# Kernel optimization log

Measured on AMD Instinct MI355X. Metric: run time of the kernel, lower is better.

## Reference

```python
import jax, jax.numpy as jnp
import numpy as np

B, N_TOTAL, IN_CH, N_SUB, E, OUT_CH = 4096, 500, 8, 77, 400, 2
EPS = 1e-12


def _glorot(key, shape, scale=0.05):
    return jax.random.normal(key, shape, dtype=jnp.float32) * scale


def setup_inputs() -> dict:
    key = jax.random.key(0)
    ks = jax.random.split(key, 16)
    x = jax.random.normal(ks[0], (B, N_TOTAL, IN_CH), dtype=jnp.float32)
    n_id = jax.random.randint(ks[1], (N_SUB,), 0, N_TOTAL)
    edge_index = jax.random.randint(ks[2], (2, E), 0, N_SUB)
    return {
        "x": x, "n_id": n_id, "edge_index": edge_index,
        # SAGEConv weights: concat doubles the input dim
        "W1": _glorot(ks[3], (2 * IN_CH, 64)), "b1": jnp.zeros((64,), jnp.float32),
        "W2": _glorot(ks[4], (2 * 64, 256)),   "b2": jnp.zeros((256,), jnp.float32),
        "W3": _glorot(ks[5], (2 * 256, 512)),  "b3": jnp.zeros((512,), jnp.float32),
        # MLP head
        "L1w": _glorot(ks[6], (512 * N_SUB, 1024), 0.01), "L1b": jnp.zeros((1024,), jnp.float32),
        "L2w": _glorot(ks[7], (1024, 218)), "L2b": jnp.zeros((218,), jnp.float32),
        "L3w": _glorot(ks[8], (218, OUT_CH)), "L3b": jnp.zeros((OUT_CH,), jnp.float32),
    }


def sage_conv(x, edge_index, W, b):
    # x: [B, N_SUB, C]; edge_index: [2, E], local ids in [0, N_SUB)
    # PyG<=1.3 SAGEConv: remove self loops, add self loops, mean aggregate,
    # concat [x, aggr], linear, L2 normalize.
    src, dst = edge_index[0], edge_index[1]
    valid = (src != dst)
    vmask = valid.astype(x.dtype)
    msgs = x[:, src, :] * vmask[None, :, None]                       # [B, E, C]
    seg = jax.vmap(lambda m: jax.ops.segment_sum(m, dst, num_segments=N_SUB))(msgs)
    counts = jax.ops.segment_sum(vmask, dst, num_segments=N_SUB)     # [N_SUB]
    aggr = (seg + x) / (counts + 1.0)[None, :, None]                 # self loop included
    h = jnp.concatenate([x, aggr], axis=-1) @ W + b
    norm = jnp.linalg.norm(h, axis=-1, keepdims=True)
    return h / jnp.maximum(norm, EPS)


def reference(x, n_id, edge_index, W1, b1, W2, b2, W3, b3,
              L1w, L1b, L2w, L2b, L3w, L3b):
    xt = x[:, n_id, :]                                               # [B, 77, 8]
    xt = jax.nn.relu(sage_conv(xt, edge_index, W1, b1))              # [B, 77, 64]
    xt = jax.nn.relu(sage_conv(xt, edge_index, W2, b2))              # [B, 77, 256]
    xt = jax.nn.relu(sage_conv(xt, edge_index, W3, b3))              # [B, 77, 512]
    xt = xt.reshape(xt.shape[0], -1)                                 # [B, 39424]
    xt = jax.nn.relu(xt @ L1w + L1b)
    xt = jax.nn.relu(xt @ L2w + L2b)
    return xt @ L3w + L3b                                            # [B, 2]
```

## Files before the change

### kernel.cpp

```cpp
#include <hip/hip_runtime.h>
#include <hip/hip_bf16.h>
#include <stdint.h>

typedef unsigned short u16;
typedef __attribute__((ext_vector_type(8))) short bf16x8_t;
typedef __attribute__((ext_vector_type(4))) float f32x4_t;

#define B_SZ   4096
#define N_TOT  500
#define IN_CH  8
#define NS     77
#define NE     400
#define L2_OUT 218

#define AS1C(p) ((const __attribute__((address_space(1))) void*)(p))
#define AS3(p)  ((__attribute__((address_space(3))) void*)(p))

__device__ inline u16 f2b(float f) {
  union { float f; uint32_t u; } v; v.f = f;
  uint32_t r = v.u + 0x7FFFu + ((v.u >> 16) & 1u);
  return (u16)(r >> 16);
}
__device__ inline float b2f(u16 h) {
  union { uint32_t u; float f; } v; v.u = ((uint32_t)h) << 16; return v.f;
}

__global__ void k_setup(const int* __restrict__ ei, int* __restrict__ coff,
                        int* __restrict__ csrc, float* __restrict__ inv) {
  if (threadIdx.x != 0 || blockIdx.x != 0) return;
  int cnt[NS], cur[NS];
  for (int i = 0; i < NS; ++i) cnt[i] = 0;
  const int* src = ei; const int* dst = ei + NE;
  for (int e = 0; e < NE; ++e) if (src[e] != dst[e]) cnt[dst[e]]++;
  int acc = 0;
  for (int i = 0; i < NS; ++i) {
    coff[i] = acc; cur[i] = acc; acc += cnt[i];
    inv[i] = 1.0f / (float)(cnt[i] + 1);
  }
  coff[NS] = acc;
  for (int e = 0; e < NE; ++e) if (src[e] != dst[e]) csrc[cur[dst[e]]++] = src[e];
}

__global__ void k_wt(const float* __restrict__ W, u16* __restrict__ Wt,
                     int K, int Nsrc, int Ndst) {
  __shared__ float t[32][33];
  int nk = K / 32;
  int bk = blockIdx.x % nk, bn = blockIdx.x / nk;
  int r = threadIdx.x >> 3, c4 = (threadIdx.x & 7) * 4;
  int gn = bn * 32 + c4;
  const float* src = &W[(size_t)(bk * 32 + r) * Nsrc + gn];
  if (gn + 3 < Nsrc) {
    float4 v = *(const float4*)src;
    t[r][c4] = v.x; t[r][c4+1] = v.y; t[r][c4+2] = v.z; t[r][c4+3] = v.w;
  } else {
    #pragma unroll
    for (int j = 0; j < 4; ++j) t[r][c4 + j] = (gn + j < Nsrc) ? src[j] : 0.f;
  }
  __syncthreads();
  ushort4 o;
  o.x = f2b(t[c4+0][r]); o.y = f2b(t[c4+1][r]);
  o.z = f2b(t[c4+2][r]); o.w = f2b(t[c4+3][r]);
  *(ushort4*)&Wt[(size_t)(bn * 32 + r) * K + bk * 32 + c4] = o;
}

__global__ __launch_bounds__(256)
void k_front(const float* __restrict__ x, const int* __restrict__ nid,
             const float* __restrict__ W1, const float* __restrict__ b1,
             const int* __restrict__ coff, const int* __restrict__ csrc,
             const float* __restrict__ invc,
             u16* __restrict__ h1, u16* __restrict__ ag1) {
  __shared__ float Ws[16 * 64];
  __shared__ float bs[64];
  __shared__ float xs[NS * 8];
  __shared__ float ac[NS * 16];
  __shared__ u16  hn[NS * 64];
  __shared__ int soff[NS + 1];
  __shared__ int ssrc[NE];
  __shared__ float sinv[NS];
  __shared__ int snid[NS];
  const int b = blockIdx.x, t = threadIdx.x;

  ((float4*)Ws)[t] = ((const float4*)W1)[t];
  if (t < 64) bs[t] = b1[t];
  if (t < NS) { snid[t] = nid[t]; sinv[t] = invc[t]; }
  if (t < NS + 1) soff[t] = coff[t];
  for (int i = t; i < NE; i += 256) ssrc[i] = csrc[i];
  __syncthreads();

  if (t < 2 * NS) {
    int i = t >> 1, p = t & 1;
    float4 v = *(const float4*)(x + ((size_t)b * N_TOT + snid[i]) * IN_CH + p * 4);
    *(float4*)&xs[i * 8 + p * 4] = v;
  }
  __syncthreads();

  if (t < NS) {
    float s[8];
    #pragma unroll
    for (int c = 0; c < 8; ++c) { s[c] = xs[t * 8 + c]; ac[t * 16 + c] = s[c]; }
    for (int e = soff[t]; e < soff[t + 1]; ++e) {
      int sb = ssrc[e] * 8;
      #pragma unroll
      for (int c = 0; c < 8; ++c) s[c] += xs[sb + c];
    }
    float iv = sinv[t];
    #pragma unroll
    for (int c = 0; c < 8; ++c) ac[t * 16 + 8 + c] = s[c] * iv;
  }
  __syncthreads();

  const int w = t >> 6, lane = t & 63;
  for (int i = w; i < NS; i += 4) {
    float acc = bs[lane];
    #pragma unroll
    for (int k = 0; k < 16; ++k) acc += ac[i * 16 + k] * Ws[k * 64 + lane];
    float ss = acc * acc;
    #pragma unroll
    for (int d = 1; d < 64; d <<= 1) ss += __shfl_xor(ss, d);
    float rn = 1.0f / fmaxf(sqrtf(ss), 1e-12f);
    u16 hv = f2b(fmaxf(acc * rn, 0.f));
    hn[i * 64 + lane] = hv;
    h1[((size_t)b * NS + i) * 64 + lane] = hv;
  }
  __syncthreads();
  for (int i = w; i < NS; i += 4) {
    float s = b2f(hn[i * 64 + lane]);
    for (int e = soff[i]; e < soff[i + 1]; ++e) s += b2f(hn[ssrc[e] * 64 + lane]);
    ag1[((size_t)b * NS + i) * 64 + lane] = f2b(s * sinv[i]);
  }
}

template<int C>
__global__ __launch_bounds__(256)
void k_norm_aggr(u16* __restrict__ h, u16* __restrict__ ag,
                 const int* __restrict__ coff, const int* __restrict__ csrc,
                 const float* __restrict__ invc) {
  __shared__ u16 sh[NS * C];
  __shared__ int soff[NS + 1];
  __shared__ int ssrc[NE];
  __shared__ float sinv[NS];
  const int b = blockIdx.x, t = threadIdx.x;
  const ushort4* hb4 = (const ushort4*)(h + (size_t)b * NS * C);
  ushort4* sh4 = (ushort4*)sh;
  for (int i4 = t; i4 < NS * C / 4; i4 += 256) sh4[i4] = hb4[i4];
  for (int i = t; i < NS + 1; i += 256) soff[i] = coff[i];
  for (int i = t; i < NE; i += 256) ssrc[i] = csrc[i];
  for (int i = t; i < NS; i += 256) sinv[i] = invc[i];
  __syncthreads();
  const int w = t >> 6, lane = t & 63;
  constexpr int PER = C / 64;
  ushort4* hb4o = (ushort4*)(h + (size_t)b * NS * C);
  for (int i = w; i < NS; i += 4) {
    float v[PER]; float ss = 0.f;
    #pragma unroll
    for (int p = 0; p < PER / 4; ++p) {
      ushort4 r = *(ushort4*)&sh[i * C + lane * PER + p * 4];
      v[p*4+0] = b2f(r.x); v[p*4+1] = b2f(r.y); v[p*4+2] = b2f(r.z); v[p*4+3] = b2f(r.w);
    }
    #pragma unroll
    for (int p = 0; p < PER; ++p) ss += v[p] * v[p];
    #pragma unroll
    for (int d = 1; d < 64; d <<= 1) ss += __shfl_xor(ss, d);
    float rn = 1.0f / fmaxf(sqrtf(ss), 1e-12f);
    #pragma unroll
    for (int p = 0; p < PER / 4; ++p) {
      ushort4 o;
      o.x = f2b(fmaxf(v[p*4+0] * rn, 0.f)); o.y = f2b(fmaxf(v[p*4+1] * rn, 0.f));
      o.z = f2b(fmaxf(v[p*4+2] * rn, 0.f)); o.w = f2b(fmaxf(v[p*4+3] * rn, 0.f));
      *(ushort4*)&sh[i * C + lane * PER + p * 4] = o;
      hb4o[(i * C + lane * PER + p * 4) / 4] = o;
    }
  }
  __syncthreads();
  ushort4* ab4 = (ushort4*)(ag + (size_t)b * NS * C);
  for (int i = w; i < NS; i += 4) {
    #pragma unroll
    for (int p = 0; p < PER / 4; ++p) {
      int c0 = lane * PER + p * 4;
      ushort4 sv = *(ushort4*)&sh[i * C + c0];
      float s0 = b2f(sv.x), s1 = b2f(sv.y), s2 = b2f(sv.z), s3 = b2f(sv.w);
      for (int e = soff[i]; e < soff[i + 1]; ++e) {
        ushort4 nv = *(ushort4*)&sh[ssrc[e] * C + c0];
        s0 += b2f(nv.x); s1 += b2f(nv.y); s2 += b2f(nv.z); s3 += b2f(nv.w);
      }
      float iv = sinv[i];
      ushort4 o; o.x = f2b(s0 * iv); o.y = f2b(s1 * iv); o.z = f2b(s2 * iv); o.w = f2b(s3 * iv);
      ab4[(i * C + c0) / 4] = o;
    }
  }
}

template<int C>
__global__ void k_normrelu(u16* __restrict__ h) {
  const int row = blockIdx.x * 4 + (threadIdx.x >> 6);
  const int lane = threadIdx.x & 63;
  constexpr int PER = C / 64;
  u16* hr = h + (size_t)row * C;
  float v[PER];
  #pragma unroll
  for (int p = 0; p < PER / 4; ++p) {
    ushort4 r = *(const ushort4*)(hr + lane * PER + p * 4);
    v[p*4+0] = b2f(r.x); v[p*4+1] = b2f(r.y); v[p*4+2] = b2f(r.z); v[p*4+3] = b2f(r.w);
  }
  float ss = 0.f;
  #pragma unroll
  for (int j = 0; j < PER; ++j) ss += v[j] * v[j];
  #pragma unroll
  for (int d = 1; d < 64; d <<= 1) ss += __shfl_xor(ss, d);
  float rn = 1.0f / fmaxf(sqrtf(ss), 1e-12f);
  #pragma unroll
  for (int p = 0; p < PER / 4; ++p) {
    ushort4 o;
    o.x = f2b(fmaxf(v[p*4+0] * rn, 0.f)); o.y = f2b(fmaxf(v[p*4+1] * rn, 0.f));
    o.z = f2b(fmaxf(v[p*4+2] * rn, 0.f)); o.w = f2b(fmaxf(v[p*4+3] * rn, 0.f));
    *(ushort4*)(hr + lane * PER + p * 4) = o;
  }
}

template<int MODE, bool CONCAT>
__global__ __launch_bounds__(256)
void k_mfma(const u16* __restrict__ A, const u16* __restrict__ A2,
            const u16* __restrict__ Bt, const float* __restrict__ bias,
            void* __restrict__ Cv, int N, int K, int CIN,
            int kPerSplit, int Mtot, int NCOLS) {
  __shared__ u16 As[2][128 * 32];
  __shared__ u16 Bs[2][128 * 32];
  const int t = threadIdx.x;
  const int gx = gridDim.x, gy = gridDim.y;
  const int nwg = gx * gy;
  const int orig = blockIdx.y * gx + blockIdx.x;
  const int q = nwg >> 3, r8 = nwg & 7;
  const int xcd = orig & 7, jj = orig >> 3;
  const int swzb = (xcd < r8 ? xcd * (q + 1) : r8 * (q + 1) + (xcd - r8) * q) + jj;
  const int mt_i = swzb / gy, nt_i = swzb - mt_i * gy;
  const int row0 = mt_i * 128, col0 = nt_i * 128;
  const int split = blockIdx.z;
  const int kbeg = split * kPerSplit;
  const int w = t >> 6, l = t & 63;
  const int wm = w >> 1, wn = w & 1;
  const int lr = l & 15, ls = l >> 4;
  const int s_row = t >> 2;
  const int s_c = ((t & 3) ^ ((t >> 3) & 3)) * 8;
  const int lsw = (ls ^ ((lr >> 1) & 3)) * 8;

  f32x4_t acc[4][4];
  #pragma unroll
  for (int i = 0; i < 4; ++i)
    #pragma unroll
    for (int j = 0; j < 4; ++j) acc[i][j] = (f32x4_t){0.f, 0.f, 0.f, 0.f};

  auto stage = [&](int buf, int k0) {
    const u16* abase; int astride, koff;
    if constexpr (CONCAT) {
      astride = CIN;
      if (k0 < CIN) { abase = A; koff = k0; } else { abase = A2; koff = k0 - CIN; }
    } else { abase = A; astride = K; koff = k0; }
    const u16* ga0 = abase + (size_t)(row0 + s_row) * astride + koff + s_c;
    const u16* ga1 = abase + (size_t)(row0 + 64 + s_row) * astride + koff + s_c;
    u16* la = &As[buf][w * 512];
    __builtin_amdgcn_global_load_lds(AS1C(ga0), AS3(la), 16, 0, 0);
    __builtin_amdgcn_global_load_lds(AS1C(ga1), AS3(la + 2048), 16, 0, 0);
    const u16* gb0 = Bt + (size_t)(col0 + s_row) * K + k0 + s_c;
    const u16* gb1 = Bt + (size_t)(col0 + 64 + s_row) * K + k0 + s_c;
    u16* lb = &Bs[buf][w * 512];
    __builtin_amdgcn_global_load_lds(AS1C(gb0), AS3(lb), 16, 0, 0);
    __builtin_amdgcn_global_load_lds(AS1C(gb1), AS3(lb + 2048), 16, 0, 0);
  };

  const int nsteps = kPerSplit / 32;
  stage(0, kbeg);
  __syncthreads();
  for (int s = 0; s < nsteps; ++s) {
    const int buf = s & 1;
    if (s + 1 < nsteps) stage(buf ^ 1, kbeg + (s + 1) * 32);
    bf16x8_t af[4], bfr[4];
    #pragma unroll
    for (int f = 0; f < 4; ++f) {
      af[f]  = *(const bf16x8_t*)&As[buf][(wm * 64 + f * 16 + lr) * 32 + lsw];
      bfr[f] = *(const bf16x8_t*)&Bs[buf][(wn * 64 + f * 16 + lr) * 32 + lsw];
    }
    #pragma unroll
    for (int i = 0; i < 4; ++i)
      #pragma unroll
      for (int j = 0; j < 4; ++j)
        acc[i][j] = __builtin_amdgcn_mfma_f32_16x16x32_bf16(af[i], bfr[j], acc[i][j], 0, 0, 0);
    __syncthreads();
  }

  const int rbase = ls * 4;
  #pragma unroll
  for (int j = 0; j < 4; ++j) {
    const int c = col0 + wn * 64 + j * 16 + lr;
    float bv = 0.f;
    if constexpr (MODE == 0) bv = bias[c];
    if constexpr (MODE == 2) bv = (c < NCOLS) ? bias[c] : 0.f;
    #pragma unroll
    for (int i = 0; i < 4; ++i) {
      const int r0 = row0 + wm * 64 + i * 16 + rbase;
      if constexpr (MODE == 0) {
        u16* C = (u16*)Cv;
        #pragma unroll
        for (int rr = 0; rr < 4; ++rr)
          C[(size_t)(r0 + rr) * N + c] = f2b(acc[i][j][rr] + bv);
      } else if constexpr (MODE == 1) {
        float* P = (float*)Cv + (size_t)split * Mtot * N;
        #pragma unroll
        for (int rr = 0; rr < 4; ++rr)
          P[(size_t)(r0 + rr) * N + c] = acc[i][j][rr];
      } else {
        if (c < NCOLS) {
          float* C = (float*)Cv;
          #pragma unroll
          for (int rr = 0; rr < 4; ++rr)
            C[(size_t)(r0 + rr) * NCOLS + c] = fmaxf(acc[i][j][rr] + bv, 0.f);
        }
      }
    }
  }
}

__global__ void k_red4(const float* __restrict__ P, const float* __restrict__ bias,
                       u16* __restrict__ y, int MN) {
  int i = blockIdx.x * 256 + threadIdx.x;
  if (i * 4 >= MN) return;
  const float4* p = (const float4*)P;
  int stride = MN / 4;
  float4 a = p[i], b = p[i + stride], c = p[i + 2 * stride], d = p[i + 3 * stride];
  float4 bv = *(const float4*)&bias[(i * 4) & 1023];
  ushort4 o;
  o.x = f2b(fmaxf(a.x + b.x + c.x + d.x + bv.x, 0.f));
  o.y = f2b(fmaxf(a.y + b.y + c.y + d.y + bv.y, 0.f));
  o.z = f2b(fmaxf(a.z + b.z + c.z + d.z + bv.z, 0.f));
  o.w = f2b(fmaxf(a.w + b.w + c.w + d.w + bv.w, 0.f));
  *(ushort4*)&y[i * 4] = o;
}

__global__ void k_l3(const float* __restrict__ y2, const float* __restrict__ w,
                     const float* __restrict__ b, float* __restrict__ out, int nrows) {
  int idx = blockIdx.x * 256 + threadIdx.x;
  if (idx >= nrows * 2) return;
  int o = idx & 1, row = idx >> 1;
  const float* yr = y2 + (size_t)row * L2_OUT;
  float s = b[o];
  for (int k = 0; k < L2_OUT; ++k) s += yr[k] * w[k * 2 + o];
  out[idx] = s;
}

extern "C" void kernel_launch(void* const* d_in, const int* in_sizes, int n_in,
                              void* d_out, int out_size, void* d_ws, size_t ws_size,
                              hipStream_t stream) {
  const float* x   = (const float*)d_in[0];
  const int*   nid = (const int*)d_in[1];
  const int*   ei  = (const int*)d_in[2];
  const float* W1  = (const float*)d_in[3];  const float* b1 = (const float*)d_in[4];
  const float* W2  = (const float*)d_in[5];  const float* b2 = (const float*)d_in[6];
  const float* W3  = (const float*)d_in[7];  const float* b3 = (const float*)d_in[8];
  const float* L1w = (const float*)d_in[9];  const float* L1b = (const float*)d_in[10];
  const float* L2w = (const float*)d_in[11]; const float* L2b = (const float*)d_in[12];
  const float* L3w = (const float*)d_in[13]; const float* L3b = (const float*)d_in[14];
  float* out = (float*)d_out;

  char* ws = (char*)d_ws;
  u16* Wt2  = (u16*)ws;
  u16* Wt3  = (u16*)(ws + 65536);
  u16* WtL1 = (u16*)(ws + 589824);
  u16* WtL2 = (u16*)(ws + 81330176);
  size_t WOFF = 81854464;
  int*   coff = (int*)(ws + WOFF);
  int*   csrc = coff + 80;
  float* invc = (float*)(csrc + 400);
  size_t CHUNK0 = WOFF + 4096;

  int Bc = 4096;
  while (Bc > 128 && CHUNK0 + (size_t)Bc * 157696 > ws_size) Bc >>= 1;

  char* r1 = ws + CHUNK0;
  char* r2 = r1 + (size_t)Bc * 39424;
  char* r3 = r2 + (size_t)Bc * 39424;

  k_setup<<<1, 64, 0, stream>>>(ei, coff, csrc, invc);
  k_wt<<<(128/32)*(256/32),    256, 0, stream>>>(W2,  Wt2,  128,   256,  256);
  k_wt<<<(512/32)*(512/32),    256, 0, stream>>>(W3,  Wt3,  512,   512,  512);
  k_wt<<<(39424/32)*(1024/32), 256, 0, stream>>>(L1w, WtL1, 39424, 1024, 1024);
  k_wt<<<(1024/32)*(256/32),   256, 0, stream>>>(L2w, WtL2, 1024,  218,  256);

  for (int b0 = 0; b0 < B_SZ; b0 += Bc) {
    const int nb = Bc;
    const int rows = nb * NS;
    const int mt = rows / 128;
    u16* h1  = (u16*)r2;
    u16* ag1 = (u16*)r3;
    u16* h2  = (u16*)r1;
    u16* ag2 = (u16*)r2;
    u16* h3  = (u16*)r3;
    u16* y1b = (u16*)r1;
    float* Pc  = (float*)(r1 + (size_t)nb * 4096);
    float* y2c = (float*)r2;
    const float* xb = x + (size_t)b0 * N_TOT * IN_CH;

    k_front<<<nb, 256, 0, stream>>>(xb, nid, W1, b1, coff, csrc, invc, h1, ag1);

    k_mfma<0, true><<<dim3(mt, 2, 1), 256, 0, stream>>>(
        h1, ag1, Wt2, b2, h2, 256, 128, 64, 128, rows, 0);
    k_norm_aggr<256><<<nb, 256, 0, stream>>>(h2, ag2, coff, csrc, invc);

    k_mfma<0, true><<<dim3(mt, 4, 1), 256, 0, stream>>>(
        h2, ag2, Wt3, b3, h3, 512, 512, 256, 512, rows, 0);
    k_normrelu<512><<<rows / 4, 256, 0, stream>>>(h3);

    k_mfma<1, false><<<dim3(nb / 128, 8, 4), 256, 0, stream>>>(
        h3, nullptr, WtL1, nullptr, Pc, 1024, 39424, 0, 9856, nb, 0);
    k_red4<<<nb, 256, 0, stream>>>(Pc, L1b, y1b, nb * 1024);

    k_mfma<2, false><<<dim3(nb / 128, 2, 1), 256, 0, stream>>>(
        y1b, nullptr, WtL2, L2b, y2c, 256, 1024, 0, 1024, nb, L2_OUT);

    k_l3<<<(nb * 2 + 255) / 256, 256, 0, stream>>>(y2c, L3w, L3b, out + (size_t)b0 * 2, nb);
  }
}
```

Before: 1.487 ms.

## Fuse L2-norm and ReLU into SAGE layer GEMM epilogues with full-row tiles

Adds a GEMM kernel whose tile spans the full output width (64 rows by all 256 or 512 columns), so the per-row L2 norm and ReLU are applied in the epilogue via a cross-wave shared-memory reduction. This removes the separate normalise pass over h2 and h3 and its extra global read and write. The aggregation kernel now only aggregates. It also parallelises the layer-1 aggregation across channels and makes the final 218-to-2 layer use one wavefront per row with shuffle reductions. The wider tiles carry more accumulators per thread, which raises register pressure, and the smaller 64-row M tile gives less reuse of each staged B tile.

```diff
diff --git a/kernel.cpp b/kernel.cpp
--- a/kernel.cpp
+++ b/kernel.cpp
@@ -94,18 +94,12 @@
   }
   __syncthreads();
 
-  if (t < NS) {
-    float s[8];
-    #pragma unroll
-    for (int c = 0; c < 8; ++c) { s[c] = xs[t * 8 + c]; ac[t * 16 + c] = s[c]; }
-    for (int e = soff[t]; e < soff[t + 1]; ++e) {
-      int sb = ssrc[e] * 8;
-      #pragma unroll
-      for (int c = 0; c < 8; ++c) s[c] += xs[sb + c];
-    }
-    float iv = sinv[t];
-    #pragma unroll
-    for (int c = 0; c < 8; ++c) ac[t * 16 + 8 + c] = s[c] * iv;
+  for (int idx = t; idx < NS * 8; idx += 256) {
+    int i = idx >> 3, c = idx & 7;
+    float s = xs[i * 8 + c];
+    ac[i * 16 + c] = s;
+    for (int e = soff[i]; e < soff[i + 1]; ++e) s += xs[ssrc[e] * 8 + c];
+    ac[i * 16 + 8 + c] = s * sinv[i];
   }
   __syncthreads();
 
@@ -132,9 +126,9 @@
 
 template<int C>
 __global__ __launch_bounds__(256)
-void k_norm_aggr(u16* __restrict__ h, u16* __restrict__ ag,
-                 const int* __restrict__ coff, const int* __restrict__ csrc,
-                 const float* __restrict__ invc) {
+void k_aggr(const u16* __restrict__ h, u16* __restrict__ ag,
+            const int* __restrict__ coff, const int* __restrict__ csrc,
+            const float* __restrict__ invc) {
   __shared__ u16 sh[NS * C];
   __shared__ int soff[NS + 1];
   __shared__ int ssrc[NE];
@@ -147,74 +141,116 @@
   for (int i = t; i < NE; i += 256) ssrc[i] = csrc[i];
   for (int i = t; i < NS; i += 256) sinv[i] = invc[i];
   __syncthreads();
-  const int w = t >> 6, lane = t & 63;
-  constexpr int PER = C / 64;
-  ushort4* hb4o = (ushort4*)(h + (size_t)b * NS * C);
-  for (int i = w; i < NS; i += 4) {
-    float v[PER]; float ss = 0.f;
-    #pragma unroll
-    for (int p = 0; p < PER / 4; ++p) {
-      ushort4 r = *(ushort4*)&sh[i * C + lane * PER + p * 4];
-      v[p*4+0] = b2f(r.x); v[p*4+1] = b2f(r.y); v[p*4+2] = b2f(r.z); v[p*4+3] = b2f(r.w);
-    }
-    #pragma unroll
-    for (int p = 0; p < PER; ++p) ss += v[p] * v[p];
-    #pragma unroll
-    for (int d = 1; d < 64; d <<= 1) ss += __shfl_xor(ss, d);
-    float rn = 1.0f / fmaxf(sqrtf(ss), 1e-12f);
-    #pragma unroll
-    for (int p = 0; p < PER / 4; ++p) {
-      ushort4 o;
-      o.x = f2b(fmaxf(v[p*4+0] * rn, 0.f)); o.y = f2b(fmaxf(v[p*4+1] * rn, 0.f));
-      o.z = f2b(fmaxf(v[p*4+2] * rn, 0.f)); o.w = f2b(fmaxf(v[p*4+3] * rn, 0.f));
-      *(ushort4*)&sh[i * C + lane * PER + p * 4] = o;
-      hb4o[(i * C + lane * PER + p * 4) / 4] = o;
-    }
-  }
-  __syncthreads();
   ushort4* ab4 = (ushort4*)(ag + (size_t)b * NS * C);
-  for (int i = w; i < NS; i += 4) {
-    #pragma unroll
-    for (int p = 0; p < PER / 4; ++p) {
-      int c0 = lane * PER + p * 4;
-      ushort4 sv = *(ushort4*)&sh[i * C + c0];
-      float s0 = b2f(sv.x), s1 = b2f(sv.y), s2 = b2f(sv.z), s3 = b2f(sv.w);
-      for (int e = soff[i]; e < soff[i + 1]; ++e) {
-        ushort4 nv = *(ushort4*)&sh[ssrc[e] * C + c0];
-        s0 += b2f(nv.x); s1 += b2f(nv.y); s2 += b2f(nv.z); s3 += b2f(nv.w);
-      }
-      float iv = sinv[i];
-      ushort4 o; o.x = f2b(s0 * iv); o.y = f2b(s1 * iv); o.z = f2b(s2 * iv); o.w = f2b(s3 * iv);
-      ab4[(i * C + c0) / 4] = o;
-    }
-  }
-}
-
-template<int C>
-__global__ void k_normrelu(u16* __restrict__ h) {
-  const int row = blockIdx.x * 4 + (threadIdx.x >> 6);
-  const int lane = threadIdx.x & 63;
-  constexpr int PER = C / 64;
-  u16* hr = h + (size_t)row * C;
-  float v[PER];
-  #pragma unroll
-  for (int p = 0; p < PER / 4; ++p) {
-    ushort4 r = *(const ushort4*)(hr + lane * PER + p * 4);
-    v[p*4+0] = b2f(r.x); v[p*4+1] = b2f(r.y); v[p*4+2] = b2f(r.z); v[p*4+3] = b2f(r.w);
-  }
-  float ss = 0.f;
-  #pragma unroll
-  for (int j = 0; j < PER; ++j) ss += v[j] * v[j];
-  #pragma unroll
-  for (int d = 1; d < 64; d <<= 1) ss += __shfl_xor(ss, d);
-  float rn = 1.0f / fmaxf(sqrtf(ss), 1e-12f);
-  #pragma unroll
-  for (int p = 0; p < PER / 4; ++p) {
-    ushort4 o;
-    o.x = f2b(fmaxf(v[p*4+0] * rn, 0.f)); o.y = f2b(fmaxf(v[p*4+1] * rn, 0.f));
-    o.z = f2b(fmaxf(v[p*4+2] * rn, 0.f)); o.w = f2b(fmaxf(v[p*4+3] * rn, 0.f));
-    *(ushort4*)(hr + lane * PER + p * 4) = o;
-  }
+  for (int i4 = t; i4 < NS * C / 4; i4 += 256) {
+    int i = i4 / (C / 4);
+    int c0 = (i4 - i * (C / 4)) * 4;
+    ushort4 sv = sh4[i4];
+    float s0 = b2f(sv.x), s1 = b2f(sv.y), s2 = b2f(sv.z), s3 = b2f(sv.w);
+    for (int e = soff[i]; e < soff[i + 1]; ++e) {
+      ushort4 nv = *(const ushort4*)&sh[ssrc[e] * C + c0];
+      s0 += b2f(nv.x); s1 += b2f(nv.y); s2 += b2f(nv.z); s3 += b2f(nv.w);
+    }
+    float iv = sinv[i];
+    ushort4 o; o.x = f2b(s0 * iv); o.y = f2b(s1 * iv); o.z = f2b(s2 * iv); o.w = f2b(s3 * iv);
+    ab4[i4] = o;
+  }
+}
+
+template<int CIN, int NC>
+__global__ __launch_bounds__(256)
+void k_mfma_norm(const u16* __restrict__ A, const u16* __restrict__ A2,
+                 const u16* __restrict__ Bt, const float* __restrict__ bias,
+                 u16* __restrict__ C) {
+  constexpr int K2 = 2 * CIN;
+  constexpr int NF = NC / 64;
+  __shared__ u16 As[2][64 * 32];
+  __shared__ u16 Bs[2][NC * 32];
+  __shared__ float sPart[64][4];
+  const int t = threadIdx.x;
+  const int nwg = gridDim.x;
+  const int orig = blockIdx.x;
+  const int q = nwg >> 3, r8 = nwg & 7;
+  const int xcd = orig & 7, jj = orig >> 3;
+  const int mt_i = (xcd < r8 ? xcd * (q + 1) : r8 * (q + 1) + (xcd - r8) * q) + jj;
+  const int row0 = mt_i * 64;
+  const int w = t >> 6, l = t & 63;
+  const int lr = l & 15, ls = l >> 4;
+  const int s_row = t >> 2;
+  const int s_c = ((t & 3) ^ ((t >> 3) & 3)) * 8;
+  const int lsw = (ls ^ ((lr >> 1) & 3)) * 8;
+
+  f32x4_t acc[4][NF];
+  #pragma unroll
+  for (int i = 0; i < 4; ++i)
+    #pragma unroll
+    for (int j = 0; j < NF; ++j) acc[i][j] = (f32x4_t){0.f, 0.f, 0.f, 0.f};
+
+  auto stage = [&](int buf, int k0) {
+    const u16* abase; int koff;
+    if (k0 < CIN) { abase = A; koff = k0; } else { abase = A2; koff = k0 - CIN; }
+    const u16* ga = abase + (size_t)(row0 + s_row) * CIN + koff + s_c;
+    __builtin_amdgcn_global_load_lds(AS1C(ga), AS3(&As[buf][w * 512]), 16, 0, 0);
+    #pragma unroll
+    for (int c = 0; c < NC / 64; ++c) {
+      const u16* gb = Bt + (size_t)(c * 64 + s_row) * K2 + k0 + s_c;
+      __builtin_amdgcn_global_load_lds(AS1C(gb), AS3(&Bs[buf][c * 2048 + w * 512]), 16, 0, 0);
+    }
+  };
+
+  constexpr int nsteps = K2 / 32;
+  stage(0, 0);
+  __syncthreads();
+  for (int s = 0; s < nsteps; ++s) {
+    const int buf = s & 1;
+    if (s + 1 < nsteps) stage(buf ^ 1, (s + 1) * 32);
+    bf16x8_t af[4], bfr[NF];
+    #pragma unroll
+    for (int f = 0; f < 4; ++f)
+      af[f] = *(const bf16x8_t*)&As[buf][(f * 16 + lr) * 32 + lsw];
+    #pragma unroll
+    for (int j = 0; j < NF; ++j)
+      bfr[j] = *(const bf16x8_t*)&Bs[buf][(w * (NC / 4) + j * 16 + lr) * 32 + lsw];
+    #pragma unroll
+    for (int i = 0; i < 4; ++i)
+      #pragma unroll
+      for (int j = 0; j < NF; ++j)
+        acc[i][j] = __builtin_amdgcn_mfma_f32_16x16x32_bf16(af[i], bfr[j], acc[i][j], 0, 0, 0);
+    __syncthreads();
+  }
+
+  #pragma unroll
+  for (int j = 0; j < NF; ++j) {
+    float bv = bias[w * (NC / 4) + j * 16 + lr];
+    #pragma unroll
+    for (int i = 0; i < 4; ++i)
+      #pragma unroll
+      for (int rr = 0; rr < 4; ++rr) acc[i][j][rr] += bv;
+  }
+  #pragma unroll
+  for (int i = 0; i < 4; ++i)
+    #pragma unroll
+    for (int rr = 0; rr < 4; ++rr) {
+      float ss = 0.f;
+      #pragma unroll
+      for (int j = 0; j < NF; ++j) ss += acc[i][j][rr] * acc[i][j][rr];
+      #pragma unroll
+      for (int d = 1; d < 16; d <<= 1) ss += __shfl_xor(ss, d);
+      if (lr == 0) sPart[i * 16 + ls * 4 + rr][w] = ss;
+    }
+  __syncthreads();
+  #pragma unroll
+  for (int i = 0; i < 4; ++i)
+    #pragma unroll
+    for (int rr = 0; rr < 4; ++rr) {
+      const int r = i * 16 + ls * 4 + rr;
+      float ss = sPart[r][0] + sPart[r][1] + sPart[r][2] + sPart[r][3];
+      float rn = 1.0f / fmaxf(sqrtf(ss), 1e-12f);
+      #pragma unroll
+      for (int j = 0; j < NF; ++j)
+        C[(size_t)(row0 + r) * NC + w * (NC / 4) + j * 16 + lr] =
+            f2b(fmaxf(acc[i][j][rr] * rn, 0.f));
+    }
 }
 
 template<int MODE, bool CONCAT>
@@ -292,17 +328,11 @@
   for (int j = 0; j < 4; ++j) {
     const int c = col0 + wn * 64 + j * 16 + lr;
     float bv = 0.f;
-    if constexpr (MODE == 0) bv = bias[c];
     if constexpr (MODE == 2) bv = (c < NCOLS) ? bias[c] : 0.f;
     #pragma unroll
     for (int i = 0; i < 4; ++i) {
       const int r0 = row0 + wm * 64 + i * 16 + rbase;
-      if constexpr (MODE == 0) {
-        u16* C = (u16*)Cv;
-        #pragma unroll
-        for (int rr = 0; rr < 4; ++rr)
-          C[(size_t)(r0 + rr) * N + c] = f2b(acc[i][j][rr] + bv);
-      } else if constexpr (MODE == 1) {
+      if constexpr (MODE == 1) {
         float* P = (float*)Cv + (size_t)split * Mtot * N;
         #pragma unroll
         for (int rr = 0; rr < 4; ++rr)
@@ -337,13 +367,18 @@
 
 __global__ void k_l3(const float* __restrict__ y2, const float* __restrict__ w,
                      const float* __restrict__ b, float* __restrict__ out, int nrows) {
-  int idx = blockIdx.x * 256 + threadIdx.x;
-  if (idx >= nrows * 2) return;
-  int o = idx & 1, row = idx >> 1;
+  const int row = blockIdx.x * 4 + (threadIdx.x >> 6);
+  const int lane = threadIdx.x & 63;
+  if (row >= nrows) return;
   const float* yr = y2 + (size_t)row * L2_OUT;
-  float s = b[o];
-  for (int k = 0; k < L2_OUT; ++k) s += yr[k] * w[k * 2 + o];
-  out[idx] = s;
+  float s0 = 0.f, s1 = 0.f;
+  for (int k = lane; k < L2_OUT; k += 64) {
+    float v = yr[k];
+    s0 += v * w[k * 2]; s1 += v * w[k * 2 + 1];
+  }
+  #pragma unroll
+  for (int d = 1; d < 64; d <<= 1) { s0 += __shfl_xor(s0, d); s1 += __shfl_xor(s1, d); }
+  if (lane == 0) { out[(size_t)row * 2] = s0 + b[0]; out[(size_t)row * 2 + 1] = s1 + b[1]; }
 }
 
 extern "C" void kernel_launch(void* const* d_in, const int* in_sizes, int n_in,
@@ -387,7 +422,6 @@
   for (int b0 = 0; b0 < B_SZ; b0 += Bc) {
     const int nb = Bc;
     const int rows = nb * NS;
-    const int mt = rows / 128;
     u16* h1  = (u16*)r2;
     u16* ag1 = (u16*)r3;
     u16* h2  = (u16*)r1;
@@ -400,13 +434,10 @@
 
     k_front<<<nb, 256, 0, stream>>>(xb, nid, W1, b1, coff, csrc, invc, h1, ag1);
 
-    k_mfma<0, true><<<dim3(mt, 2, 1), 256, 0, stream>>>(
-        h1, ag1, Wt2, b2, h2, 256, 128, 64, 128, rows, 0);
-    k_norm_aggr<256><<<nb, 256, 0, stream>>>(h2, ag2, coff, csrc, invc);
-
-    k_mfma<0, true><<<dim3(mt, 4, 1), 256, 0, stream>>>(
-        h2, ag2, Wt3, b3, h3, 512, 512, 256, 512, rows, 0);
-    k_normrelu<512><<<rows / 4, 256, 0, stream>>>(h3);
+    k_mfma_norm<64, 256><<<rows / 64, 256, 0, stream>>>(h1, ag1, Wt2, b2, h2);
+    k_aggr<256><<<nb, 256, 0, stream>>>(h2, ag2, coff, csrc, invc);
+
+    k_mfma_norm<256, 512><<<rows / 64, 256, 0, stream>>>(h2, ag2, Wt3, b3, h3);
 
     k_mfma<1, false><<<dim3(nb / 128, 8, 4), 256, 0, stream>>>(
         h3, nullptr, WtL1, nullptr, Pc, 1024, 39424, 0, 9856, nb, 0);
@@ -415,6 +446,6 @@
     k_mfma<2, false><<<dim3(nb / 128, 2, 1), 256, 0, stream>>>(
         y1b, nullptr, WtL2, L2b, y2c, 256, 1024, 0, 1024, nb, L2_OUT);
 
-    k_l3<<<(nb * 2 + 255) / 256, 256, 0, stream>>>(y2c, L3w, L3b, out + (size_t)b0 * 2, nb);
-  }
-}
+    k_l3<<<nb / 4, 256, 0, stream>>>(y2c, L3w, L3b, out + (size_t)b0 * 2, nb);
+  }
+}
```

New measurement: 1.655 ms. +11.3%, slower.

## Add 256x256 8-wave MFMA GEMM with 4-stage LDS pipeline for layer3 and L1

Applied to the files above, without the earlier changes.

Introduces a new 512-thread GEMM kernel with 256x256 output tiles, a 4-deep global_load_lds pipeline, XCD-aware block swizzle and setprio around MFMA bursts. It replaces the previous 128-tile kernel for the third SAGE linear and the large split-K L1 head. This raises arithmetic intensity per tile and should cut operand reloads. The front aggregation is also parallelised across channels, and the final 2-output layer now uses one wavefront per row with shuffle reductions. Larger tiles use more registers and LDS, allowing one block per CU, and the minimum chunk size rises to 256.

```diff
diff --git a/kernel.cpp b/kernel.cpp
--- a/kernel.cpp
+++ b/kernel.cpp
@@ -94,18 +94,12 @@
   }
   __syncthreads();
 
-  if (t < NS) {
-    float s[8];
-    #pragma unroll
-    for (int c = 0; c < 8; ++c) { s[c] = xs[t * 8 + c]; ac[t * 16 + c] = s[c]; }
-    for (int e = soff[t]; e < soff[t + 1]; ++e) {
-      int sb = ssrc[e] * 8;
-      #pragma unroll
-      for (int c = 0; c < 8; ++c) s[c] += xs[sb + c];
-    }
-    float iv = sinv[t];
-    #pragma unroll
-    for (int c = 0; c < 8; ++c) ac[t * 16 + 8 + c] = s[c] * iv;
+  for (int idx = t; idx < NS * 8; idx += 256) {
+    int i = idx >> 3, c = idx & 7;
+    float s = xs[i * 8 + c];
+    ac[i * 16 + c] = s;
+    for (int e = soff[i]; e < soff[i + 1]; ++e) s += xs[ssrc[e] * 8 + c];
+    ac[i * 16 + 8 + c] = s * sinv[i];
   }
   __syncthreads();
 
@@ -302,11 +296,6 @@
         #pragma unroll
         for (int rr = 0; rr < 4; ++rr)
           C[(size_t)(r0 + rr) * N + c] = f2b(acc[i][j][rr] + bv);
-      } else if constexpr (MODE == 1) {
-        float* P = (float*)Cv + (size_t)split * Mtot * N;
-        #pragma unroll
-        for (int rr = 0; rr < 4; ++rr)
-          P[(size_t)(r0 + rr) * N + c] = acc[i][j][rr];
       } else {
         if (c < NCOLS) {
           float* C = (float*)Cv;
@@ -314,6 +303,125 @@
           for (int rr = 0; rr < 4; ++rr)
             C[(size_t)(r0 + rr) * NCOLS + c] = fmaxf(acc[i][j][rr] + bv, 0.f);
         }
+      }
+    }
+  }
+}
+
+template<int MODE, bool CONCAT>
+__global__ __launch_bounds__(512, 1)
+void k_mfma8(const u16* __restrict__ A, const u16* __restrict__ A2,
+             const u16* __restrict__ Bt, const float* __restrict__ bias,
+             void* __restrict__ Cv, int N, int K, int CIN,
+             int kPerSplit, int Mtot) {
+  __shared__ u16 As[4][256 * 32];
+  __shared__ u16 Bs[4][256 * 32];
+  const int t = threadIdx.x;
+  const int gx = gridDim.x, gy = gridDim.y;
+  const int nwg = gx * gy;
+  const int orig = blockIdx.y * gx + blockIdx.x;
+  const int q = nwg >> 3, r8 = nwg & 7;
+  const int xcd = orig & 7, jj = orig >> 3;
+  const int swzb = (xcd < r8 ? xcd * (q + 1) : r8 * (q + 1) + (xcd - r8) * q) + jj;
+  const int mt_i = swzb / gy, nt_i = swzb - mt_i * gy;
+  const int row0 = mt_i * 256, col0 = nt_i * 256;
+  const int split = blockIdx.z;
+  const int kbeg = split * kPerSplit;
+  const int w = t >> 6, l = t & 63;
+  const int wm = w >> 2, wn = w & 3;
+  const int lr = l & 15, ls = l >> 4;
+  const int s_row = t >> 2;
+  const int s_c = ((t & 3) ^ ((t >> 3) & 3)) * 8;
+  const int lsw = (ls ^ ((lr >> 1) & 3)) * 8;
+
+  f32x4_t acc[8][4];
+  #pragma unroll
+  for (int i = 0; i < 8; ++i)
+    #pragma unroll
+    for (int j = 0; j < 4; ++j) acc[i][j] = (f32x4_t){0.f, 0.f, 0.f, 0.f};
+
+  auto stageA = [&](int Tt) {
+    const int k0 = kbeg + Tt * 32;
+    const u16* abase; int astride, koff;
+    if constexpr (CONCAT) {
+      astride = CIN;
+      if (k0 < CIN) { abase = A; koff = k0; } else { abase = A2; koff = k0 - CIN; }
+    } else { abase = A; astride = K; koff = k0; }
+    u16* dst = &As[Tt & 3][w * 512];
+    __builtin_amdgcn_global_load_lds(
+        AS1C(abase + (size_t)(row0 + s_row) * astride + koff + s_c), AS3(dst), 16, 0, 0);
+    __builtin_amdgcn_global_load_lds(
+        AS1C(abase + (size_t)(row0 + 128 + s_row) * astride + koff + s_c), AS3(dst + 4096), 16, 0, 0);
+  };
+  auto stageB = [&](int Tt) {
+    const int k0 = kbeg + Tt * 32;
+    u16* dst = &Bs[Tt & 3][w * 512];
+    __builtin_amdgcn_global_load_lds(
+        AS1C(Bt + (size_t)(col0 + s_row) * K + k0 + s_c), AS3(dst), 16, 0, 0);
+    __builtin_amdgcn_global_load_lds(
+        AS1C(Bt + (size_t)(col0 + 128 + s_row) * K + k0 + s_c), AS3(dst + 4096), 16, 0, 0);
+  };
+
+  const int NT = kPerSplit / 32;
+  const int pre = NT < 3 ? NT : 3;
+  for (int p = 0; p < pre; ++p) { stageA(p); stageB(p); }
+
+  for (int T = 0; T < NT; ++T) {
+    const int rem = NT - 1 - T;
+    if (rem >= 2)      asm volatile("s_waitcnt vmcnt(8)" ::: "memory");
+    else if (rem == 1) asm volatile("s_waitcnt vmcnt(4)" ::: "memory");
+    else               asm volatile("s_waitcnt vmcnt(0)" ::: "memory");
+    __builtin_amdgcn_s_barrier();
+    asm volatile("" ::: "memory");
+
+    if (T + 3 < NT) stageA(T + 3);
+    const u16* AB = &As[T & 3][0];
+    const u16* BB = &Bs[T & 3][0];
+    bf16x8_t bf[4], af[4];
+    #pragma unroll
+    for (int g = 0; g < 4; ++g)
+      bf[g] = *(const bf16x8_t*)&BB[(wn * 64 + g * 16 + lr) * 32 + lsw];
+    #pragma unroll
+    for (int f = 0; f < 4; ++f)
+      af[f] = *(const bf16x8_t*)&AB[(wm * 128 + f * 16 + lr) * 32 + lsw];
+    if (T + 3 < NT) stageB(T + 3);
+    __builtin_amdgcn_s_setprio(1);
+    #pragma unroll
+    for (int i = 0; i < 4; ++i)
+      #pragma unroll
+      for (int g = 0; g < 4; ++g)
+        acc[i][g] = __builtin_amdgcn_mfma_f32_16x16x32_bf16(af[i], bf[g], acc[i][g], 0, 0, 0);
+    __builtin_amdgcn_s_setprio(0);
+    #pragma unroll
+    for (int f = 0; f < 4; ++f)
+      af[f] = *(const bf16x8_t*)&AB[(wm * 128 + 64 + f * 16 + lr) * 32 + lsw];
+    __builtin_amdgcn_s_setprio(1);
+    #pragma unroll
+    for (int i = 0; i < 4; ++i)
+      #pragma unroll
+      for (int g = 0; g < 4; ++g)
+        acc[4 + i][g] = __builtin_amdgcn_mfma_f32_16x16x32_bf16(af[i], bf[g], acc[4 + i][g], 0, 0, 0);
+    __builtin_amdgcn_s_setprio(0);
+  }
+
+  #pragma unroll
+  for (int j = 0; j < 4; ++j) {
+    const int c = col0 + wn * 64 + j * 16 + lr;
+    float bv = 0.f;
+    if constexpr (MODE == 0) bv = bias[c];
+    #pragma unroll
+    for (int i = 0; i < 8; ++i) {
+      const int r0 = row0 + wm * 128 + i * 16 + ls * 4;
+      if constexpr (MODE == 0) {
+        u16* C = (u16*)Cv;
+        #pragma unroll
+        for (int rr = 0; rr < 4; ++rr)
+          C[(size_t)(r0 + rr) * N + c] = f2b(acc[i][j][rr] + bv);
+      } else {
+        float* P = (float*)Cv + (size_t)split * Mtot * N;
+        #pragma unroll
+        for (int rr = 0; rr < 4; ++rr)
+          P[(size_t)(r0 + rr) * N + c] = acc[i][j][rr];
       }
     }
   }
@@ -337,13 +445,18 @@
 
 __global__ void k_l3(const float* __restrict__ y2, const float* __restrict__ w,
                      const float* __restrict__ b, float* __restrict__ out, int nrows) {
-  int idx = blockIdx.x * 256 + threadIdx.x;
-  if (idx >= nrows * 2) return;
-  int o = idx & 1, row = idx >> 1;
+  const int row = blockIdx.x * 4 + (threadIdx.x >> 6);
+  const int lane = threadIdx.x & 63;
+  if (row >= nrows) return;
   const float* yr = y2 + (size_t)row * L2_OUT;
-  float s = b[o];
-  for (int k = 0; k < L2_OUT; ++k) s += yr[k] * w[k * 2 + o];
-  out[idx] = s;
+  float s0 = 0.f, s1 = 0.f;
+  for (int k = lane; k < L2_OUT; k += 64) {
+    float v = yr[k];
+    s0 += v * w[k * 2]; s1 += v * w[k * 2 + 1];
+  }
+  #pragma unroll
+  for (int d = 1; d < 64; d <<= 1) { s0 += __shfl_xor(s0, d); s1 += __shfl_xor(s1, d); }
+  if (lane == 0) { out[(size_t)row * 2] = s0 + b[0]; out[(size_t)row * 2 + 1] = s1 + b[1]; }
 }
 
 extern "C" void kernel_launch(void* const* d_in, const int* in_sizes, int n_in,
@@ -372,7 +485,7 @@
   size_t CHUNK0 = WOFF + 4096;
 
   int Bc = 4096;
-  while (Bc > 128 && CHUNK0 + (size_t)Bc * 157696 > ws_size) Bc >>= 1;
+  while (Bc > 256 && CHUNK0 + (size_t)Bc * 157696 > ws_size) Bc >>= 1;
 
   char* r1 = ws + CHUNK0;
   char* r2 = r1 + (size_t)Bc * 39424;
@@ -404,17 +517,17 @@
         h1, ag1, Wt2, b2, h2, 256, 128, 64, 128, rows, 0);
     k_norm_aggr<256><<<nb, 256, 0, stream>>>(h2, ag2, coff, csrc, invc);
 
-    k_mfma<0, true><<<dim3(mt, 4, 1), 256, 0, stream>>>(
-        h2, ag2, Wt3, b3, h3, 512, 512, 256, 512, rows, 0);
+    k_mfma8<0, true><<<dim3(rows / 256, 2, 1), 512, 0, stream>>>(
+        h2, ag2, Wt3, b3, h3, 512, 512, 256, 512, rows);
     k_normrelu<512><<<rows / 4, 256, 0, stream>>>(h3);
 
-    k_mfma<1, false><<<dim3(nb / 128, 8, 4), 256, 0, stream>>>(
-        h3, nullptr, WtL1, nullptr, Pc, 1024, 39424, 0, 9856, nb, 0);
+    k_mfma8<1, false><<<dim3(nb / 256, 4, 4), 512, 0, stream>>>(
+        h3, nullptr, WtL1, nullptr, Pc, 1024, 39424, 0, 9856, nb);
     k_red4<<<nb, 256, 0, stream>>>(Pc, L1b, y1b, nb * 1024);
 
     k_mfma<2, false><<<dim3(nb / 128, 2, 1), 256, 0, stream>>>(
         y1b, nullptr, WtL2, L2b, y2c, 256, 1024, 0, 1024, nb, L2_OUT);
 
-    k_l3<<<(nb * 2 + 255) / 256, 256, 0, stream>>>(y2c, L3w, L3b, out + (size_t)b0 * 2, nb);
-  }
-}
+    k_l3<<<nb / 4, 256, 0, stream>>>(y2c, L3w, L3b, out + (size_t)b0 * 2, nb);
+  }
+}
```

Result: slower. 1.695 ms (+14.0%).

## Fuse L2-normalize and ReLU of layer 3 into L1 GEMM A-tile staging

Applied to the files above, without the earlier changes.

Replaces the in-place normalize+ReLU pass over h3 with a kernel that only computes per-row inverse norms. The big L1 GEMM then loads A tiles through registers, applying relu and scaling before writing to LDS. This removes a full write-back of the largest activation tensor, at the cost of losing async global-to-LDS loads for A in that GEMM. It also parallelizes the first-layer aggregation across channels and makes the final 2-output layer warp-per-row with shuffles.

```diff
diff --git a/kernel.cpp b/kernel.cpp
--- a/kernel.cpp
+++ b/kernel.cpp
@@ -94,18 +94,12 @@
   }
   __syncthreads();
 
-  if (t < NS) {
-    float s[8];
-    #pragma unroll
-    for (int c = 0; c < 8; ++c) { s[c] = xs[t * 8 + c]; ac[t * 16 + c] = s[c]; }
-    for (int e = soff[t]; e < soff[t + 1]; ++e) {
-      int sb = ssrc[e] * 8;
-      #pragma unroll
-      for (int c = 0; c < 8; ++c) s[c] += xs[sb + c];
-    }
-    float iv = sinv[t];
-    #pragma unroll
-    for (int c = 0; c < 8; ++c) ac[t * 16 + 8 + c] = s[c] * iv;
+  for (int idx = t; idx < NS * 8; idx += 256) {
+    int i = idx >> 3, c = idx & 7;
+    float s = xs[i * 8 + c];
+    ac[i * 16 + c] = s;
+    for (int e = soff[i]; e < soff[i + 1]; ++e) s += xs[ssrc[e] * 8 + c];
+    ac[i * 16 + 8 + c] = s * sinv[i];
   }
   __syncthreads();
 
@@ -191,36 +185,28 @@
 }
 
 template<int C>
-__global__ void k_normrelu(u16* __restrict__ h) {
+__global__ void k_norms(const u16* __restrict__ h, float* __restrict__ rn_out) {
   const int row = blockIdx.x * 4 + (threadIdx.x >> 6);
   const int lane = threadIdx.x & 63;
   constexpr int PER = C / 64;
-  u16* hr = h + (size_t)row * C;
-  float v[PER];
+  const u16* hr = h + (size_t)row * C;
+  float ss = 0.f;
   #pragma unroll
   for (int p = 0; p < PER / 4; ++p) {
     ushort4 r = *(const ushort4*)(hr + lane * PER + p * 4);
-    v[p*4+0] = b2f(r.x); v[p*4+1] = b2f(r.y); v[p*4+2] = b2f(r.z); v[p*4+3] = b2f(r.w);
-  }
-  float ss = 0.f;
-  #pragma unroll
-  for (int j = 0; j < PER; ++j) ss += v[j] * v[j];
+    float a = b2f(r.x), b = b2f(r.y), c = b2f(r.z), d = b2f(r.w);
+    ss += a * a + b * b + c * c + d * d;
+  }
   #pragma unroll
   for (int d = 1; d < 64; d <<= 1) ss += __shfl_xor(ss, d);
-  float rn = 1.0f / fmaxf(sqrtf(ss), 1e-12f);
-  #pragma unroll
-  for (int p = 0; p < PER / 4; ++p) {
-    ushort4 o;
-    o.x = f2b(fmaxf(v[p*4+0] * rn, 0.f)); o.y = f2b(fmaxf(v[p*4+1] * rn, 0.f));
-    o.z = f2b(fmaxf(v[p*4+2] * rn, 0.f)); o.w = f2b(fmaxf(v[p*4+3] * rn, 0.f));
-    *(ushort4*)(hr + lane * PER + p * 4) = o;
-  }
-}
-
-template<int MODE, bool CONCAT>
+  if (lane == 0) rn_out[row] = 1.0f / fmaxf(sqrtf(ss), 1e-12f);
+}
+
+template<int MODE, bool CONCAT, bool ANORM>
 __global__ __launch_bounds__(256)
 void k_mfma(const u16* __restrict__ A, const u16* __restrict__ A2,
             const u16* __restrict__ Bt, const float* __restrict__ bias,
+            const float* __restrict__ rnorm,
             void* __restrict__ Cv, int N, int K, int CIN,
             int kPerSplit, int Mtot, int NCOLS) {
   __shared__ u16 As[2][128 * 32];
@@ -249,7 +235,39 @@
     #pragma unroll
     for (int j = 0; j < 4; ++j) acc[i][j] = (f32x4_t){0.f, 0.f, 0.f, 0.f};
 
-  auto stage = [&](int buf, int k0) {
+  uint4 ra0, ra1; float n0 = 0.f, n1 = 0.f;
+
+  auto loadA_regs = [&](int k0) {
+    ra0 = *(const uint4*)(A + (size_t)(row0 + s_row) * K + k0 + s_c);
+    ra1 = *(const uint4*)(A + (size_t)(row0 + 64 + s_row) * K + k0 + s_c);
+    const int node = k0 >> 9;
+    n0 = rnorm[(row0 + s_row) * NS + node];
+    n1 = rnorm[(row0 + 64 + s_row) * NS + node];
+  };
+  auto writeA_lds = [&](int buf) {
+    u16* la = &As[buf][w * 512 + l * 8];
+    ushort4 o0, o1;
+    o0.x = f2b(fmaxf(b2f((u16)(ra0.x & 0xffff)), 0.f) * n0);
+    o0.y = f2b(fmaxf(b2f((u16)(ra0.x >> 16)),    0.f) * n0);
+    o0.z = f2b(fmaxf(b2f((u16)(ra0.y & 0xffff)), 0.f) * n0);
+    o0.w = f2b(fmaxf(b2f((u16)(ra0.y >> 16)),    0.f) * n0);
+    o1.x = f2b(fmaxf(b2f((u16)(ra0.z & 0xffff)), 0.f) * n0);
+    o1.y = f2b(fmaxf(b2f((u16)(ra0.z >> 16)),    0.f) * n0);
+    o1.z = f2b(fmaxf(b2f((u16)(ra0.w & 0xffff)), 0.f) * n0);
+    o1.w = f2b(fmaxf(b2f((u16)(ra0.w >> 16)),    0.f) * n0);
+    *(ushort4*)la = o0; *(ushort4*)(la + 4) = o1;
+    u16* lb = la + 2048;
+    o0.x = f2b(fmaxf(b2f((u16)(ra1.x & 0xffff)), 0.f) * n1);
+    o0.y = f2b(fmaxf(b2f((u16)(ra1.x >> 16)),    0.f) * n1);
+    o0.z = f2b(fmaxf(b2f((u16)(ra1.y & 0xffff)), 0.f) * n1);
+    o0.w = f2b(fmaxf(b2f((u16)(ra1.y >> 16)),    0.f) * n1);
+    o1.x = f2b(fmaxf(b2f((u16)(ra1.z & 0xffff)), 0.f) * n1);
+    o1.y = f2b(fmaxf(b2f((u16)(ra1.z >> 16)),    0.f) * n1);
+    o1.z = f2b(fmaxf(b2f((u16)(ra1.w & 0xffff)), 0.f) * n1);
+    o1.w = f2b(fmaxf(b2f((u16)(ra1.w >> 16)),    0.f) * n1);
+    *(ushort4*)lb = o0; *(ushort4*)(lb + 4) = o1;
+  };
+  auto stageA_gld = [&](int buf, int k0) {
     const u16* abase; int astride, koff;
     if constexpr (CONCAT) {
       astride = CIN;
@@ -260,6 +278,8 @@
     u16* la = &As[buf][w * 512];
     __builtin_amdgcn_global_load_lds(AS1C(ga0), AS3(la), 16, 0, 0);
     __builtin_amdgcn_global_load_lds(AS1C(ga1), AS3(la + 2048), 16, 0, 0);
+  };
+  auto stageB_gld = [&](int buf, int k0) {
     const u16* gb0 = Bt + (size_t)(col0 + s_row) * K + k0 + s_c;
     const u16* gb1 = Bt + (size_t)(col0 + 64 + s_row) * K + k0 + s_c;
     u16* lb = &Bs[buf][w * 512];
@@ -268,11 +288,20 @@
   };
 
   const int nsteps = kPerSplit / 32;
-  stage(0, kbeg);
+  if constexpr (ANORM) {
+    loadA_regs(kbeg); stageB_gld(0, kbeg); writeA_lds(0);
+  } else {
+    stageA_gld(0, kbeg); stageB_gld(0, kbeg);
+  }
   __syncthreads();
   for (int s = 0; s < nsteps; ++s) {
     const int buf = s & 1;
-    if (s + 1 < nsteps) stage(buf ^ 1, kbeg + (s + 1) * 32);
+    const bool more = (s + 1 < nsteps);
+    if (more) {
+      const int nk = kbeg + (s + 1) * 32;
+      if constexpr (ANORM) { loadA_regs(nk); stageB_gld(buf ^ 1, nk); }
+      else { stageA_gld(buf ^ 1, nk); stageB_gld(buf ^ 1, nk); }
+    }
     bf16x8_t af[4], bfr[4];
     #pragma unroll
     for (int f = 0; f < 4; ++f) {
@@ -284,6 +313,7 @@
       #pragma unroll
       for (int j = 0; j < 4; ++j)
         acc[i][j] = __builtin_amdgcn_mfma_f32_16x16x32_bf16(af[i], bfr[j], acc[i][j], 0, 0, 0);
+    if constexpr (ANORM) { if (more) writeA_lds(buf ^ 1); }
     __syncthreads();
   }
 
@@ -337,13 +367,18 @@
 
 __global__ void k_l3(const float* __restrict__ y2, const float* __restrict__ w,
                      const float* __restrict__ b, float* __restrict__ out, int nrows) {
-  int idx = blockIdx.x * 256 + threadIdx.x;
-  if (idx >= nrows * 2) return;
-  int o = idx & 1, row = idx >> 1;
+  const int row = blockIdx.x * 4 + (threadIdx.x >> 6);
+  const int lane = threadIdx.x & 63;
+  if (row >= nrows) return;
   const float* yr = y2 + (size_t)row * L2_OUT;
-  float s = b[o];
-  for (int k = 0; k < L2_OUT; ++k) s += yr[k] * w[k * 2 + o];
-  out[idx] = s;
+  float s0 = 0.f, s1 = 0.f;
+  for (int k = lane; k < L2_OUT; k += 64) {
+    float v = yr[k];
+    s0 += v * w[k * 2]; s1 += v * w[k * 2 + 1];
+  }
+  #pragma unroll
+  for (int d = 1; d < 64; d <<= 1) { s0 += __shfl_xor(s0, d); s1 += __shfl_xor(s1, d); }
+  if (lane == 0) { out[(size_t)row * 2] = s0 + b[0]; out[(size_t)row * 2 + 1] = s1 + b[1]; }
 }
 
 extern "C" void kernel_launch(void* const* d_in, const int* in_sizes, int n_in,
@@ -372,11 +407,12 @@
   size_t CHUNK0 = WOFF + 4096;
 
   int Bc = 4096;
-  while (Bc > 128 && CHUNK0 + (size_t)Bc * 157696 > ws_size) Bc >>= 1;
+  while (Bc > 128 && CHUNK0 + (size_t)Bc * 158016 > ws_size) Bc >>= 1;
 
   char* r1 = ws + CHUNK0;
   char* r2 = r1 + (size_t)Bc * 39424;
   char* r3 = r2 + (size_t)Bc * 39424;
+  float* rnv = (float*)(r3 + (size_t)Bc * 78848);
 
   k_setup<<<1, 64, 0, stream>>>(ei, coff, csrc, invc);
   k_wt<<<(128/32)*(256/32),    256, 0, stream>>>(W2,  Wt2,  128,   256,  256);
@@ -400,21 +436,21 @@
 
     k_front<<<nb, 256, 0, stream>>>(xb, nid, W1, b1, coff, csrc, invc, h1, ag1);
 
-    k_mfma<0, true><<<dim3(mt, 2, 1), 256, 0, stream>>>(
-        h1, ag1, Wt2, b2, h2, 256, 128, 64, 128, rows, 0);
+    k_mfma<0, true, false><<<dim3(mt, 2, 1), 256, 0, stream>>>(
+        h1, ag1, Wt2, b2, nullptr, h2, 256, 128, 64, 128, rows, 0);
     k_norm_aggr<256><<<nb, 256, 0, stream>>>(h2, ag2, coff, csrc, invc);
 
-    k_mfma<0, true><<<dim3(mt, 4, 1), 256, 0, stream>>>(
-        h2, ag2, Wt3, b3, h3, 512, 512, 256, 512, rows, 0);
-    k_normrelu<512><<<rows / 4, 256, 0, stream>>>(h3);
-
-    k_mfma<1, false><<<dim3(nb / 128, 8, 4), 256, 0, stream>>>(
-        h3, nullptr, WtL1, nullptr, Pc, 1024, 39424, 0, 9856, nb, 0);
+    k_mfma<0, true, false><<<dim3(mt, 4, 1), 256, 0, stream>>>(
+        h2, ag2, Wt3, b3, nullptr, h3, 512, 512, 256, 512, rows, 0);
+    k_norms<512><<<rows / 4, 256, 0, stream>>>(h3, rnv);
+
+    k_mfma<1, false, true><<<dim3(nb / 128, 8, 4), 256, 0, stream>>>(
+        h3, nullptr, WtL1, nullptr, rnv, Pc, 1024, 39424, 0, 9856, nb, 0);
     k_red4<<<nb, 256, 0, stream>>>(Pc, L1b, y1b, nb * 1024);
 
-    k_mfma<2, false><<<dim3(nb / 128, 2, 1), 256, 0, stream>>>(
-        y1b, nullptr, WtL2, L2b, y2c, 256, 1024, 0, 1024, nb, L2_OUT);
-
-    k_l3<<<(nb * 2 + 255) / 256, 256, 0, stream>>>(y2c, L3w, L3b, out + (size_t)b0 * 2, nb);
-  }
-}
+    k_mfma<2, false, false><<<dim3(nb / 128, 2, 1), 256, 0, stream>>>(
+        y1b, nullptr, WtL2, L2b, nullptr, y2c, 256, 1024, 0, 1024, nb, L2_OUT);
+
+    k_l3<<<nb / 4, 256, 0, stream>>>(y2c, L3w, L3b, out + (size_t)b0 * 2, nb);
+  }
+}
```

New measurement: 1.662 ms. 11.8% more time.
